# Optimization experiments

Measured on AMD Instinct MI355X. Metric: run time of the kernel, lower is better.

Reference implementation:

```python
import jax, jax.numpy as jnp
import numpy as np

B, C, H, W = 8, 192, 128, 128
NH, WS, PS = 6, 8, 8
HD = C // NH
SCALE = HD ** -0.5

def _rel_pos_log(ws):
    # log-spaced signed relative coordinates, [N, N, 2]
    coords = np.stack(np.meshgrid(np.arange(ws), np.arange(ws), indexing='ij'))
    cf = coords.reshape(2, -1)
    rp = (cf[:, :, None] - cf[:, None, :]).transpose(1, 2, 0).astype(np.float32)
    return jnp.asarray(np.sign(rp) * np.log1p(np.abs(rp)))

def setup_inputs() -> dict:
    key = jax.random.key(0)
    ks = jax.random.split(key, 8)
    s = 0.02
    return {
        'x': jax.random.normal(ks[0], (B, C, H, W), jnp.float32),
        'V_w': jax.random.normal(ks[1], (C, C), jnp.float32) * s,
        'V_b': jnp.zeros((C,), jnp.float32),
        'QK_w': jax.random.normal(ks[2], (2 * C, C), jnp.float32) * s,
        'QK_b': jnp.zeros((2 * C,), jnp.float32),
        'proj_w': jax.random.normal(ks[3], (C, C), jnp.float32) * s,
        'proj_b': jnp.zeros((C,), jnp.float32),
        'meta_w1': jax.random.normal(ks[4], (2, 256), jnp.float32) * s,
        'meta_b1': jnp.zeros((256,), jnp.float32),
        'meta_w2': jax.random.normal(ks[5], (256, NH), jnp.float32) * s,
        'meta_b2': jnp.zeros((NH,), jnp.float32),
    }

def reference(x, V_w, V_b, QK_w, QK_b, proj_w, proj_b, meta_w1, meta_b1, meta_w2, meta_b2):
    N = WS * WS
    # 1x1 convs for V and QK
    v = jnp.einsum('bchw,oc->bohw', x, V_w) + V_b[None, :, None, None]
    qk = jnp.einsum('bchw,oc->bohw', x, QK_w) + QK_b[None, :, None, None]
    qkv = jnp.concatenate([qk, v], axis=1)  # [B, 3C, H, W]
    # window partition -> [B * nW, N, 3C]
    t = qkv.transpose(0, 2, 3, 1).reshape(B, H // WS, WS, W // WS, WS, 3 * C)
    wins = t.transpose(0, 1, 3, 2, 4, 5).reshape(-1, N, 3 * C)
    B_ = wins.shape[0]
    qkv3 = wins.reshape(B_, N, 3, NH, HD).transpose(2, 0, 3, 1, 4)
    q, k, vv = qkv3[0] * SCALE, qkv3[1], qkv3[2]  # [B_, NH, N, HD]
    # FFT cross-modulation of q and k over the 8x8 window grid (c = N/64 = 1)
    cg = N // (PS * PS)
    qp = q.reshape(B_, NH, cg, PS, PS, HD).transpose(0, 1, 2, 5, 3, 4)
    kp = k.reshape(B_, NH, cg, PS, PS, HD).transpose(0, 1, 2, 5, 3, 4)
    o = jnp.fft.irfft2(jnp.fft.rfft2(qp) * jnp.fft.rfft2(kp), s=(PS, PS))
    o = o.transpose(0, 1, 2, 4, 5, 3).reshape(B_, NH, N, HD)
    # relative position bias from meta MLP on log-spaced coords
    rp = _rel_pos_log(WS)  # [N, N, 2]
    bias = jax.nn.relu(rp @ meta_w1 + meta_b1) @ meta_w2 + meta_b2  # [N, N, NH]
    bias = bias.transpose(2, 0, 1)  # [NH, N, N]
    attn = jnp.einsum('bhnd,bhmd->bhnm', o, vv) + bias[None]
    attn = jax.nn.softmax(attn, axis=-1)
    y = jnp.einsum('bhnm,bhmd->bhnd', attn, vv).transpose(0, 2, 1, 3).reshape(B_, N, C)
    # window reverse -> [B, C, H, W]
    y = y.reshape(B, H // WS, W // WS, WS, WS, C).transpose(0, 1, 3, 2, 4, 5).reshape(B, H, W, C)
    y = y.transpose(0, 3, 1, 2)
    return jnp.einsum('bchw,oc->bohw', y, proj_w) + proj_b[None, :, None, None]
```

## Files before the change

### kernel.cpp

```cpp
#include <hip/hip_runtime.h>

#define SCALEQ 0.17677669529663687f

typedef __bf16 bf16x8 __attribute__((ext_vector_type(8)));
typedef float f32x4 __attribute__((ext_vector_type(4)));
typedef float f32x2 __attribute__((ext_vector_type(2)));

__device__ __forceinline__ float bflo(unsigned int u) { return __uint_as_float(u << 16); }
__device__ __forceinline__ float bfhi(unsigned int u) { return __uint_as_float(u & 0xffff0000u); }
__device__ __forceinline__ f32x2 b2x2(unsigned int u) {
    f32x2 r; r[0] = bflo(u); r[1] = bfhi(u); return r;
}
__device__ __forceinline__ unsigned short f2b(float f) {
    unsigned int u = __float_as_uint(f);
    u += 0x7fffu + ((u >> 16) & 1u);
    return (unsigned short)(u >> 16);
}

#define BUF0   0
#define QOFF   24576
#define KOFF   49152
#define POFF   24576
#define VOFF   73728
#define VTOFF  98304
#define BTOFF  122880
#define LDS_BYTES 128280

#define WS_WQKV_ELEMS 110592
#define WS_WP_OFF_EL  110592
#define WS_BT_OFF_B   294912

__device__ __forceinline__ bf16x8 ldsf(const char* p) {
    uint4 u = *(const uint4*)p;
    return __builtin_bit_cast(bf16x8, u);
}
__device__ __forceinline__ bf16x8 gldf(const unsigned short* p) {
    uint4 u = *(const uint4*)p;
    return __builtin_bit_cast(bf16x8, u);
}

__global__ void wprep_kernel(const float* __restrict__ QKw, const float* __restrict__ Vw,
                             const float* __restrict__ Pw, unsigned short* __restrict__ wsb) {
    int i = blockIdx.x * 256 + threadIdx.x;
    if (i >= 147456) return;
    if (i < WS_WQKV_ELEMS) {
        int r = i / 192, c = i - r * 192;
        float v = (r < 384) ? QKw[r * 192 + c] : Vw[(r - 384) * 192 + c];
        wsb[i] = f2b(v);
    } else {
        int j = i - WS_WQKV_ELEMS;
        wsb[WS_WP_OFF_EL + j] = f2b(Pw[j]);
    }
}

__global__ void bias_table_kernel(const float* __restrict__ Mw1, const float* __restrict__ Mb1,
                                  const float* __restrict__ Mw2, const float* __restrict__ Mb2,
                                  float* __restrict__ bias_out) {
    int t = blockIdx.x * 64 + threadIdx.x;
    if (t >= 225) return;
    int dyi = t / 15, dxi = t % 15;
    float dy = (float)(dyi - 7), dx = (float)(dxi - 7);
    float f0 = copysignf(log1pf(fabsf(dy)), dy);
    float f1 = copysignf(log1pf(fabsf(dx)), dx);
    float a0 = Mb2[0], a1 = Mb2[1], a2 = Mb2[2], a3 = Mb2[3], a4 = Mb2[4], a5 = Mb2[5];
    for (int u = 0; u < 256; ++u) {
        float hv = fmaxf(f0 * Mw1[u] + f1 * Mw1[256 + u] + Mb1[u], 0.0f);
        const float* w2 = Mw2 + u * 6;
        a0 = fmaf(hv, w2[0], a0); a1 = fmaf(hv, w2[1], a1);
        a2 = fmaf(hv, w2[2], a2); a3 = fmaf(hv, w2[3], a3);
        a4 = fmaf(hv, w2[4], a4); a5 = fmaf(hv, w2[5], a5);
    }
    float* bt = bias_out + t * 6;
    bt[0] = a0; bt[1] = a1; bt[2] = a2; bt[3] = a3; bt[4] = a4; bt[5] = a5;
}

__global__ __launch_bounds__(512, 2)
void fused_win_attn(const float* __restrict__ x,
                    const float* __restrict__ Vb, const float* __restrict__ QKb,
                    const float* __restrict__ Pb,
                    const unsigned short* __restrict__ wqkv,
                    const unsigned short* __restrict__ wp,
                    const float* __restrict__ bias_g,
                    float* __restrict__ out)
{
    extern __shared__ char smem[];
    const int t   = threadIdx.x;
    const int wv  = t >> 6;
    const int l15 = t & 15;
    const int l4  = (t >> 4) & 3;

    const int wid = ((blockIdx.x & 7) << 8) | (blockIdx.x >> 3);
    const int b   = wid >> 8;
    const int wy  = (wid >> 4) & 15;
    const int wx  = wid & 15;
    const int y0  = wy * 8, x0 = wx * 8;

    const f32x4 zz = {0.0f, 0.0f, 0.0f, 0.0f};

    {
        float* bt = (float*)(smem + BTOFF);
        for (int i = t; i < 1350; i += 512) bt[i] = bias_g[i];
    }

    {
        const float* xb = x + (size_t)b * 192 * 16384;
        #pragma unroll
        for (int i = 0; i < 6; ++i) {
            int idx = t + 512 * i;
            int c = idx >> 4, sub = idx & 15;
            int r = sub >> 1, hf = sub & 1;
            float4 v4 = *(const float4*)(xb + c * 16384 + (y0 + r) * 128 + x0 + hf * 4);
            int n0 = r * 8 + hf * 4;
            unsigned short sv[4] = {f2b(v4.x), f2b(v4.y), f2b(v4.z), f2b(v4.w)};
            #pragma unroll
            for (int e = 0; e < 4; ++e) {
                int n = n0 + e;
                *(unsigned short*)(smem + BUF0 + ((n * 384 + c * 2) ^ ((n & 7) << 4))) = sv[e];
            }
        }
    }
    __syncthreads();

    {
        const int wcol = wv & 3, wrow = wv >> 2;
        bf16x8 afr[6][2];
        #pragma unroll
        for (int ks = 0; ks < 6; ++ks)
            #pragma unroll
            for (int mtl = 0; mtl < 2; ++mtl) {
                int row = (wrow * 2 + mtl) * 16 + l15;
                afr[ks][mtl] = ldsf(smem + BUF0 + ((row * 384 + ks * 64 + l4 * 16) ^ ((row & 7) << 4)));
            }
        #pragma unroll
        for (int chunk = 0; chunk < 3; ++chunk) {
            bf16x8 bw[3][6];
            #pragma unroll
            for (int j = 0; j < 3; ++j) {
                int ob = wcol * 144 + chunk * 48 + j * 16;
                const unsigned short* wr = wqkv + (size_t)(ob + l15) * 192 + l4 * 8;
                #pragma unroll
                for (int ks = 0; ks < 6; ++ks) bw[j][ks] = gldf(wr + ks * 32);
            }
            f32x4 acc[3][2];
            #pragma unroll
            for (int j = 0; j < 3; ++j) { acc[j][0] = zz; acc[j][1] = zz; }
            #pragma unroll
            for (int ks = 0; ks < 6; ++ks)
                #pragma unroll
                for (int j = 0; j < 3; ++j)
                    #pragma unroll
                    for (int mtl = 0; mtl < 2; ++mtl)
                        acc[j][mtl] = __builtin_amdgcn_mfma_f32_16x16x32_bf16(afr[ks][mtl], bw[j][ks], acc[j][mtl], 0, 0, 0);
            #pragma unroll
            for (int j = 0; j < 3; ++j) {
                int ob  = wcol * 144 + chunk * 48 + j * 16;
                int och = ob + l15;
                float bv = (ob < 384) ? QKb[och] : Vb[och - 384];
                #pragma unroll
                for (int mtl = 0; mtl < 2; ++mtl) {
                    #pragma unroll
                    for (int rr = 0; rr < 4; ++rr) {
                        float val = acc[j][mtl][rr] + bv;
                        int tok = (wrow * 2 + mtl) * 16 + l4 * 4 + rr;
                        if (ob < 192) {
                            *(unsigned short*)(smem + QOFF + ((tok * 384 + och * 2) ^ ((tok & 7) << 4))) = f2b(val * SCALEQ);
                        } else if (ob < 384) {
                            int ch = och - 192;
                            *(unsigned short*)(smem + KOFF + ((tok * 384 + ch * 2) ^ ((tok & 7) << 4))) = f2b(val);
                        } else {
                            int ch = och - 384;
                            unsigned short hv = f2b(val);
                            *(unsigned short*)(smem + VOFF  + ((tok * 384 + ch * 2) ^ ((tok & 7) << 4))) = hv;
                            *(unsigned short*)(smem + VTOFF + ((ch * 128 + tok * 2) ^ ((ch & 7) << 4))) = hv;
                        }
                    }
                }
            }
        }
    }
    __syncthreads();

    if (t < 384) {
        const int rn = t / 48, cc = t % 48;
        const int c0b = cc * 8;
        f32x2 acc[8][2];
        #pragma unroll
        for (int cn = 0; cn < 8; ++cn) {
            acc[cn][0] = (f32x2){0.0f, 0.0f};
            acc[cn][1] = (f32x2){0.0f, 0.0f};
        }

        #pragma unroll
        for (int kh = 0; kh < 2; ++kh) {
            uint2 karr[32];
            #pragma unroll
            for (int m = 0; m < 32; ++m) {
                int row = kh * 32 + m;
                karr[m] = *(const uint2*)(smem + KOFF + ((row * 384 + c0b) ^ ((row & 7) << 4)));
            }
            #pragma unroll
            for (int mrl = 0; mrl < 4; ++mrl) {
                const int mr = kh * 4 + mrl;
                f32x2 kf[8][2];
                #pragma unroll
                for (int mc = 0; mc < 8; ++mc) {
                    uint2 kv = karr[mrl * 8 + mc];
                    kf[mc][0] = b2x2(kv.x); kf[mc][1] = b2x2(kv.y);
                }
                const int npr = (rn - mr) & 7;
                #pragma unroll
                for (int npc = 0; npc < 8; ++npc) {
                    int np = npr * 8 + npc;
                    uint2 qv = *(const uint2*)(smem + QOFF + ((np * 384 + c0b) ^ ((np & 7) << 4)));
                    f32x2 qf0 = b2x2(qv.x), qf1 = b2x2(qv.y);
                    #pragma unroll
                    for (int mc = 0; mc < 8; ++mc) {
                        int cn = (npc + mc) & 7;
                        acc[cn][0] = qf0 * kf[mc][0] + acc[cn][0];
                        acc[cn][1] = qf1 * kf[mc][1] + acc[cn][1];
                    }
                }
            }
        }
        #pragma unroll
        for (int cn = 0; cn < 8; ++cn) {
            int n = rn * 8 + cn;
            uint2 pk;
            pk.x = (unsigned int)f2b(acc[cn][0][0]) | ((unsigned int)f2b(acc[cn][0][1]) << 16);
            pk.y = (unsigned int)f2b(acc[cn][1][0]) | ((unsigned int)f2b(acc[cn][1][1]) << 16);
            *(uint2*)(smem + BUF0 + ((n * 384 + c0b) ^ ((n & 7) << 4))) = pk;
        }
    }
    __syncthreads();

    {
        const float* bt = (const float*)(smem + BTOFF);
        for (int i = 0; i < 3; ++i) {
            int u = wv * 3 + i;
            int h = u >> 2, mt = u & 3;
            int arow = mt * 16 + l15;
            bf16x8 afr = ldsf(smem + BUF0 + ((arow * 384 + h * 64 + l4 * 16) ^ ((arow & 7) << 4)));
            f32x4 acc[4];
            #pragma unroll
            for (int nt = 0; nt < 4; ++nt) {
                int brow = nt * 16 + l15;
                bf16x8 bfr = ldsf(smem + VOFF + ((brow * 384 + h * 64 + l4 * 16) ^ ((brow & 7) << 4)));
                acc[nt] = __builtin_amdgcn_mfma_f32_16x16x32_bf16(afr, bfr, zz, 0, 0, 0);
            }
            float s[4][4];
            #pragma unroll
            for (int nt = 0; nt < 4; ++nt) {
                int m = nt * 16 + l15;
                int myr = m >> 3, myc = m & 7;
                #pragma unroll
                for (int rr = 0; rr < 4; ++rr) {
                    int n = mt * 16 + l4 * 4 + rr;
                    int dy = (n >> 3) - myr + 7, dx = (n & 7) - myc + 7;
                    s[nt][rr] = acc[nt][rr] + bt[(dy * 15 + dx) * 6 + h];
                }
            }
            float inv[4];
            #pragma unroll
            for (int rr = 0; rr < 4; ++rr) {
                float m0 = fmaxf(fmaxf(s[0][rr], s[1][rr]), fmaxf(s[2][rr], s[3][rr]));
                m0 = fmaxf(m0, __shfl_xor(m0, 1));
                m0 = fmaxf(m0, __shfl_xor(m0, 2));
                m0 = fmaxf(m0, __shfl_xor(m0, 4));
                m0 = fmaxf(m0, __shfl_xor(m0, 8));
                float sm = 0.0f;
                #pragma unroll
                for (int nt = 0; nt < 4; ++nt) {
                    float p = __expf(s[nt][rr] - m0);
                    s[nt][rr] = p; sm += p;
                }
                sm += __shfl_xor(sm, 1); sm += __shfl_xor(sm, 2);
                sm += __shfl_xor(sm, 4); sm += __shfl_xor(sm, 8);
                inv[rr] = 1.0f / sm;
            }
            #pragma unroll
            for (int nt = 0; nt < 4; ++nt)
                #pragma unroll
                for (int rr = 0; rr < 4; ++rr) {
                    int n = mt * 16 + l4 * 4 + rr, m = nt * 16 + l15;
                    *(unsigned short*)(smem + POFF + h * 8192 + ((n * 128 + m * 2) ^ ((n & 7) << 4)))
                        = f2b(s[nt][rr] * inv[rr]);
                }
        }
    }
    __syncthreads();

    {
        for (int i = 0; i < 3; ++i) {
            int u = wv * 3 + i;
            int h = u >> 2, mt = u & 3;
            bf16x8 pa[2];
            #pragma unroll
            for (int ks = 0; ks < 2; ++ks) {
                int row = mt * 16 + l15;
                pa[ks] = ldsf(smem + POFF + h * 8192 + ((row * 128 + ks * 64 + l4 * 16) ^ ((row & 7) << 4)));
            }
            f32x4 acc[2];
            acc[0] = zz; acc[1] = zz;
            #pragma unroll
            for (int dt = 0; dt < 2; ++dt)
                #pragma unroll
                for (int ks = 0; ks < 2; ++ks) {
                    int ch = h * 32 + dt * 16 + l15;
                    bf16x8 bfr = ldsf(smem + VTOFF + ((ch * 128 + ks * 64 + l4 * 16) ^ ((ch & 7) << 4)));
                    acc[dt] = __builtin_amdgcn_mfma_f32_16x16x32_bf16(pa[ks], bfr, acc[dt], 0, 0, 0);
                }
            #pragma unroll
            for (int dt = 0; dt < 2; ++dt)
                #pragma unroll
                for (int rr = 0; rr < 4; ++rr) {
                    int tok = mt * 16 + l4 * 4 + rr;
                    int ch  = h * 32 + dt * 16 + l15;
                    *(unsigned short*)(smem + BUF0 + ((tok * 384 + ch * 2) ^ ((tok & 7) << 4))) = f2b(acc[dt][rr]);
                }
        }
    }
    __syncthreads();

    {
        const int wc = wv & 3, wr = wv >> 2;
        bf16x8 wfr[3][6];
        #pragma unroll
        for (int jt = 0; jt < 3; ++jt) {
            int oc = wc * 48 + jt * 16;
            const unsigned short* wr_ = wp + (size_t)(oc + l15) * 192 + l4 * 8;
            #pragma unroll
            for (int ks = 0; ks < 6; ++ks) wfr[jt][ks] = gldf(wr_ + ks * 32);
        }
        f32x4 acc[3][2];
        #pragma unroll
        for (int jt = 0; jt < 3; ++jt) { acc[jt][0] = zz; acc[jt][1] = zz; }

        #pragma unroll
        for (int ks = 0; ks < 6; ++ks) {
            bf16x8 bfr[2];
            #pragma unroll
            for (int ntl = 0; ntl < 2; ++ntl) {
                int tok = (wr * 2 + ntl) * 16 + l15;
                bfr[ntl] = ldsf(smem + BUF0 + ((tok * 384 + ks * 64 + l4 * 16) ^ ((tok & 7) << 4)));
            }
            #pragma unroll
            for (int jt = 0; jt < 3; ++jt)
                #pragma unroll
                for (int ntl = 0; ntl < 2; ++ntl)
                    acc[jt][ntl] = __builtin_amdgcn_mfma_f32_16x16x32_bf16(wfr[jt][ks], bfr[ntl], acc[jt][ntl], 0, 0, 0);
        }
        #pragma unroll
        for (int jt = 0; jt < 3; ++jt)
            #pragma unroll
            for (int rr = 0; rr < 4; ++rr) {
                int oc = wc * 48 + jt * 16 + l4 * 4 + rr;
                float pb = Pb[oc];
                float* obase = out + (size_t)(b * 192 + oc) * 16384;
                #pragma unroll
                for (int ntl = 0; ntl < 2; ++ntl) {
                    int tok = (wr * 2 + ntl) * 16 + l15;
                    obase[(y0 + (tok >> 3)) * 128 + x0 + (tok & 7)] = acc[jt][ntl][rr] + pb;
                }
            }
    }
}

extern "C" void kernel_launch(void* const* d_in, const int* in_sizes, int n_in,
                              void* d_out, int out_size, void* d_ws, size_t ws_size,
                              hipStream_t stream) {
    const float* x   = (const float*)d_in[0];
    const float* Vw  = (const float*)d_in[1];
    const float* Vb  = (const float*)d_in[2];
    const float* QKw = (const float*)d_in[3];
    const float* QKb = (const float*)d_in[4];
    const float* Pw  = (const float*)d_in[5];
    const float* Pb  = (const float*)d_in[6];
    const float* Mw1 = (const float*)d_in[7];
    const float* Mb1 = (const float*)d_in[8];
    const float* Mw2 = (const float*)d_in[9];
    const float* Mb2 = (const float*)d_in[10];
    float* outp = (float*)d_out;

    unsigned short* wsb  = (unsigned short*)d_ws;
    float* biasw = (float*)((char*)d_ws + WS_BT_OFF_B);

    wprep_kernel<<<dim3(576), dim3(256), 0, stream>>>(QKw, Vw, Pw, wsb);
    bias_table_kernel<<<dim3(4), dim3(64), 0, stream>>>(Mw1, Mb1, Mw2, Mb2, biasw);

    (void)hipFuncSetAttribute((const void*)fused_win_attn,
                              hipFuncAttributeMaxDynamicSharedMemorySize, LDS_BYTES);
    fused_win_attn<<<dim3(2048), dim3(512), LDS_BYTES, stream>>>(
        x, Vb, QKb, Pb, wsb, wsb + WS_WP_OFF_EL, biasw, outp);
}
```

Before: 333.7 us.

## Shrink LDS footprint via buffer aliasing and register-resident P/V to double occupancy

```diff
diff --git a/kernel.cpp b/kernel.cpp
--- a/kernel.cpp
+++ b/kernel.cpp
@@ -16,15 +16,15 @@
     u += 0x7fffu + ((u >> 16) & 1u);
     return (unsigned short)(u >> 16);
 }
-
-#define BUF0   0
-#define QOFF   24576
-#define KOFF   49152
-#define POFF   24576
-#define VOFF   73728
-#define VTOFF  98304
-#define BTOFF  122880
-#define LDS_BYTES 128280
+__device__ __forceinline__ unsigned int pk2(float a, float b) {
+    return (unsigned int)f2b(a) | ((unsigned int)f2b(b) << 16);
+}
+
+#define RA     0
+#define RB     24576
+#define RC     49152
+#define BTOFF  73728
+#define LDS_BYTES 79128
 
 #define WS_WQKV_ELEMS 110592
 #define WS_WP_OFF_EL  110592
@@ -74,7 +74,7 @@
     bt[0] = a0; bt[1] = a1; bt[2] = a2; bt[3] = a3; bt[4] = a4; bt[5] = a5;
 }
 
-__global__ __launch_bounds__(512, 2)
+__global__ __launch_bounds__(512, 4)
 void fused_win_attn(const float* __restrict__ x,
                     const float* __restrict__ Vb, const float* __restrict__ QKb,
                     const float* __restrict__ Pb,
@@ -115,33 +115,33 @@
             #pragma unroll
             for (int e = 0; e < 4; ++e) {
                 int n = n0 + e;
-                *(unsigned short*)(smem + BUF0 + ((n * 384 + c * 2) ^ ((n & 7) << 4))) = sv[e];
-            }
-        }
-    }
-    __syncthreads();
-
-    {
-        const int wcol = wv & 3, wrow = wv >> 2;
+                *(unsigned short*)(smem + RA + ((n * 384 + c * 2) ^ ((n & 7) << 4))) = sv[e];
+            }
+        }
+    }
+    __syncthreads();
+
+    const int wcol = wv & 3, wrow = wv >> 2;
+    unsigned int vp[3][2][2];
+    {
         bf16x8 afr[6][2];
         #pragma unroll
         for (int ks = 0; ks < 6; ++ks)
             #pragma unroll
             for (int mtl = 0; mtl < 2; ++mtl) {
                 int row = (wrow * 2 + mtl) * 16 + l15;
-                afr[ks][mtl] = ldsf(smem + BUF0 + ((row * 384 + ks * 64 + l4 * 16) ^ ((row & 7) << 4)));
-            }
-        #pragma unroll
-        for (int chunk = 0; chunk < 3; ++chunk) {
+                afr[ks][mtl] = ldsf(smem + RA + ((row * 384 + ks * 64 + l4 * 16) ^ ((row & 7) << 4)));
+            }
+        __syncthreads();
+
+        auto gemm3 = [&](int obase, f32x4 acc[3][2]) {
             bf16x8 bw[3][6];
             #pragma unroll
             for (int j = 0; j < 3; ++j) {
-                int ob = wcol * 144 + chunk * 48 + j * 16;
-                const unsigned short* wr = wqkv + (size_t)(ob + l15) * 192 + l4 * 8;
+                const unsigned short* wr = wqkv + (size_t)(obase + j * 16 + l15) * 192 + l4 * 8;
                 #pragma unroll
                 for (int ks = 0; ks < 6; ++ks) bw[j][ks] = gldf(wr + ks * 32);
             }
-            f32x4 acc[3][2];
             #pragma unroll
             for (int j = 0; j < 3; ++j) { acc[j][0] = zz; acc[j][1] = zz; }
             #pragma unroll
@@ -151,29 +151,53 @@
                     #pragma unroll
                     for (int mtl = 0; mtl < 2; ++mtl)
                         acc[j][mtl] = __builtin_amdgcn_mfma_f32_16x16x32_bf16(afr[ks][mtl], bw[j][ks], acc[j][mtl], 0, 0, 0);
+        };
+
+        {
+            f32x4 acc[3][2];
+            gemm3(wcol * 48, acc);
             #pragma unroll
             for (int j = 0; j < 3; ++j) {
-                int ob  = wcol * 144 + chunk * 48 + j * 16;
-                int och = ob + l15;
-                float bv = (ob < 384) ? QKb[och] : Vb[och - 384];
-                #pragma unroll
-                for (int mtl = 0; mtl < 2; ++mtl) {
+                int och = wcol * 48 + j * 16 + l15;
+                float bv = QKb[och];
+                #pragma unroll
+                for (int mtl = 0; mtl < 2; ++mtl)
                     #pragma unroll
                     for (int rr = 0; rr < 4; ++rr) {
-                        float val = acc[j][mtl][rr] + bv;
                         int tok = (wrow * 2 + mtl) * 16 + l4 * 4 + rr;
-                        if (ob < 192) {
-                            *(unsigned short*)(smem + QOFF + ((tok * 384 + och * 2) ^ ((tok & 7) << 4))) = f2b(val * SCALEQ);
-                        } else if (ob < 384) {
-                            int ch = och - 192;
-                            *(unsigned short*)(smem + KOFF + ((tok * 384 + ch * 2) ^ ((tok & 7) << 4))) = f2b(val);
-                        } else {
-                            int ch = och - 384;
-                            unsigned short hv = f2b(val);
-                            *(unsigned short*)(smem + VOFF  + ((tok * 384 + ch * 2) ^ ((tok & 7) << 4))) = hv;
-                            *(unsigned short*)(smem + VTOFF + ((ch * 128 + tok * 2) ^ ((ch & 7) << 4))) = hv;
-                        }
+                        *(unsigned short*)(smem + RA + ((tok * 384 + och * 2) ^ ((tok & 7) << 4)))
+                            = f2b((acc[j][mtl][rr] + bv) * SCALEQ);
                     }
+            }
+        }
+        {
+            f32x4 acc[3][2];
+            gemm3(192 + wcol * 48, acc);
+            #pragma unroll
+            for (int j = 0; j < 3; ++j) {
+                int ch = wcol * 48 + j * 16 + l15;
+                float bv = QKb[192 + ch];
+                #pragma unroll
+                for (int mtl = 0; mtl < 2; ++mtl)
+                    #pragma unroll
+                    for (int rr = 0; rr < 4; ++rr) {
+                        int tok = (wrow * 2 + mtl) * 16 + l4 * 4 + rr;
+                        *(unsigned short*)(smem + RB + ((tok * 384 + ch * 2) ^ ((tok & 7) << 4)))
+                            = f2b(acc[j][mtl][rr] + bv);
+                    }
+            }
+        }
+        {
+            f32x4 acc[3][2];
+            gemm3(384 + wcol * 48, acc);
+            #pragma unroll
+            for (int j = 0; j < 3; ++j) {
+                int ch = wcol * 48 + j * 16 + l15;
+                float bv = Vb[ch];
+                #pragma unroll
+                for (int mtl = 0; mtl < 2; ++mtl) {
+                    vp[j][mtl][0] = pk2(acc[j][mtl][0] + bv, acc[j][mtl][1] + bv);
+                    vp[j][mtl][1] = pk2(acc[j][mtl][2] + bv, acc[j][mtl][3] + bv);
                 }
             }
         }
@@ -189,14 +213,13 @@
             acc[cn][0] = (f32x2){0.0f, 0.0f};
             acc[cn][1] = (f32x2){0.0f, 0.0f};
         }
-
         #pragma unroll
         for (int kh = 0; kh < 2; ++kh) {
             uint2 karr[32];
             #pragma unroll
             for (int m = 0; m < 32; ++m) {
                 int row = kh * 32 + m;
-                karr[m] = *(const uint2*)(smem + KOFF + ((row * 384 + c0b) ^ ((row & 7) << 4)));
+                karr[m] = *(const uint2*)(smem + RB + ((row * 384 + c0b) ^ ((row & 7) << 4)));
             }
             #pragma unroll
             for (int mrl = 0; mrl < 4; ++mrl) {
@@ -211,7 +234,7 @@
                 #pragma unroll
                 for (int npc = 0; npc < 8; ++npc) {
                     int np = npr * 8 + npc;
-                    uint2 qv = *(const uint2*)(smem + QOFF + ((np * 384 + c0b) ^ ((np & 7) << 4)));
+                    uint2 qv = *(const uint2*)(smem + RA + ((np * 384 + c0b) ^ ((np & 7) << 4)));
                     f32x2 qf0 = b2x2(qv.x), qf1 = b2x2(qv.y);
                     #pragma unroll
                     for (int mc = 0; mc < 8; ++mc) {
@@ -226,78 +249,103 @@
         for (int cn = 0; cn < 8; ++cn) {
             int n = rn * 8 + cn;
             uint2 pk;
-            pk.x = (unsigned int)f2b(acc[cn][0][0]) | ((unsigned int)f2b(acc[cn][0][1]) << 16);
-            pk.y = (unsigned int)f2b(acc[cn][1][0]) | ((unsigned int)f2b(acc[cn][1][1]) << 16);
-            *(uint2*)(smem + BUF0 + ((n * 384 + c0b) ^ ((n & 7) << 4))) = pk;
-        }
-    }
-    __syncthreads();
-
+            pk.x = pk2(acc[cn][0][0], acc[cn][0][1]);
+            pk.y = pk2(acc[cn][1][0], acc[cn][1][1]);
+            *(uint2*)(smem + RC + ((n * 384 + c0b) ^ ((n & 7) << 4))) = pk;
+        }
+    }
+    __syncthreads();
+
+    {
+        #pragma unroll
+        for (int j = 0; j < 3; ++j) {
+            int ch = wcol * 48 + j * 16 + l15;
+            #pragma unroll
+            for (int mtl = 0; mtl < 2; ++mtl)
+                #pragma unroll
+                for (int pp = 0; pp < 2; ++pp) {
+                    unsigned int pk = vp[j][mtl][pp];
+                    int tok0 = (wrow * 2 + mtl) * 16 + l4 * 4 + pp * 2;
+                    *(unsigned int*)(smem + RB + ((ch * 128 + tok0 * 2) ^ ((ch & 7) << 4))) = pk;
+                    *(unsigned short*)(smem + RA + ((tok0 * 384 + ch * 2) ^ ((tok0 & 7) << 4)))
+                        = (unsigned short)(pk & 0xffffu);
+                    *(unsigned short*)(smem + RA + (((tok0 + 1) * 384 + ch * 2) ^ (((tok0 + 1) & 7) << 4)))
+                        = (unsigned short)(pk >> 16);
+                }
+        }
+    }
+    __syncthreads();
+
+    unsigned int pv[3][4][2];
     {
         const float* bt = (const float*)(smem + BTOFF);
+        #pragma unroll
         for (int i = 0; i < 3; ++i) {
             int u = wv * 3 + i;
-            int h = u >> 2, mt = u & 3;
-            int arow = mt * 16 + l15;
-            bf16x8 afr = ldsf(smem + BUF0 + ((arow * 384 + h * 64 + l4 * 16) ^ ((arow & 7) << 4)));
-            f32x4 acc[4];
-            #pragma unroll
-            for (int nt = 0; nt < 4; ++nt) {
-                int brow = nt * 16 + l15;
-                bf16x8 bfr = ldsf(smem + VOFF + ((brow * 384 + h * 64 + l4 * 16) ^ ((brow & 7) << 4)));
-                acc[nt] = __builtin_amdgcn_mfma_f32_16x16x32_bf16(afr, bfr, zz, 0, 0, 0);
-            }
+            int h = u >> 2, nt = u & 3;
+            int brow = nt * 16 + l15;
+            bf16x8 ofr = ldsf(smem + RC + ((brow * 384 + h * 64 + l4 * 16) ^ ((brow & 7) << 4)));
+            int n = nt * 16 + l15;
+            int nr = n >> 3, nc = n & 7;
             float s[4][4];
             #pragma unroll
-            for (int nt = 0; nt < 4; ++nt) {
-                int m = nt * 16 + l15;
-                int myr = m >> 3, myc = m & 7;
+            for (int mt = 0; mt < 4; ++mt) {
+                int arow = mt * 16 + l15;
+                bf16x8 vfr = ldsf(smem + RA + ((arow * 384 + h * 64 + l4 * 16) ^ ((arow & 7) << 4)));
+                f32x4 a = __builtin_amdgcn_mfma_f32_16x16x32_bf16(vfr, ofr, zz, 0, 0, 0);
                 #pragma unroll
                 for (int rr = 0; rr < 4; ++rr) {
-                    int n = mt * 16 + l4 * 4 + rr;
-                    int dy = (n >> 3) - myr + 7, dx = (n & 7) - myc + 7;
-                    s[nt][rr] = acc[nt][rr] + bt[(dy * 15 + dx) * 6 + h];
-                }
-            }
-            float inv[4];
-            #pragma unroll
-            for (int rr = 0; rr < 4; ++rr) {
-                float m0 = fmaxf(fmaxf(s[0][rr], s[1][rr]), fmaxf(s[2][rr], s[3][rr]));
-                m0 = fmaxf(m0, __shfl_xor(m0, 1));
-                m0 = fmaxf(m0, __shfl_xor(m0, 2));
-                m0 = fmaxf(m0, __shfl_xor(m0, 4));
-                m0 = fmaxf(m0, __shfl_xor(m0, 8));
-                float sm = 0.0f;
-                #pragma unroll
-                for (int nt = 0; nt < 4; ++nt) {
-                    float p = __expf(s[nt][rr] - m0);
-                    s[nt][rr] = p; sm += p;
-                }
-                sm += __shfl_xor(sm, 1); sm += __shfl_xor(sm, 2);
-                sm += __shfl_xor(sm, 4); sm += __shfl_xor(sm, 8);
-                inv[rr] = 1.0f / sm;
-            }
-            #pragma unroll
-            for (int nt = 0; nt < 4; ++nt)
+                    int m = mt * 16 + l4 * 4 + rr;
+                    int dy = nr - (m >> 3) + 7, dx = nc - (m & 7) + 7;
+                    s[mt][rr] = a[rr] + bt[(dy * 15 + dx) * 6 + h];
+                }
+            }
+            float m0 = s[0][0];
+            #pragma unroll
+            for (int mt = 0; mt < 4; ++mt)
+                #pragma unroll
+                for (int rr = 0; rr < 4; ++rr) m0 = fmaxf(m0, s[mt][rr]);
+            m0 = fmaxf(m0, __shfl_xor(m0, 16));
+            m0 = fmaxf(m0, __shfl_xor(m0, 32));
+            float sm = 0.0f;
+            #pragma unroll
+            for (int mt = 0; mt < 4; ++mt)
                 #pragma unroll
                 for (int rr = 0; rr < 4; ++rr) {
-                    int n = mt * 16 + l4 * 4 + rr, m = nt * 16 + l15;
-                    *(unsigned short*)(smem + POFF + h * 8192 + ((n * 128 + m * 2) ^ ((n & 7) << 4)))
-                        = f2b(s[nt][rr] * inv[rr]);
-                }
-        }
-    }
-    __syncthreads();
-
-    {
+                    float p = __expf(s[mt][rr] - m0);
+                    s[mt][rr] = p; sm += p;
+                }
+            sm += __shfl_xor(sm, 16);
+            sm += __shfl_xor(sm, 32);
+            float inv = 1.0f / sm;
+            #pragma unroll
+            for (int mt = 0; mt < 4; ++mt) {
+                pv[i][mt][0] = pk2(s[mt][0] * inv, s[mt][1] * inv);
+                pv[i][mt][1] = pk2(s[mt][2] * inv, s[mt][3] * inv);
+            }
+        }
+    }
+    __syncthreads();
+
+    {
+        #pragma unroll
         for (int i = 0; i < 3; ++i) {
             int u = wv * 3 + i;
-            int h = u >> 2, mt = u & 3;
-            bf16x8 pa[2];
+            int h = u >> 2, nt = u & 3;
+            bf16x8 pafr[2];
             #pragma unroll
             for (int ks = 0; ks < 2; ++ks) {
-                int row = mt * 16 + l15;
-                pa[ks] = ldsf(smem + POFF + h * 8192 + ((row * 128 + ks * 64 + l4 * 16) ^ ((row & 7) << 4)));
+                unsigned int au[4];
+                #pragma unroll
+                for (int p = 0; p < 4; ++p) {
+                    int srcl4 = (2 * l4 + (p >> 1)) & 3;
+                    int src = srcl4 * 16 + l15;
+                    unsigned int v0 = (unsigned int)__shfl((int)pv[i][2 * ks][p & 1], src, 64);
+                    unsigned int v1 = (unsigned int)__shfl((int)pv[i][2 * ks + 1][p & 1], src, 64);
+                    au[p] = (l4 & 2) ? v1 : v0;
+                }
+                uint4 u4 = {au[0], au[1], au[2], au[3]};
+                pafr[ks] = __builtin_bit_cast(bf16x8, u4);
             }
             f32x4 acc[2];
             acc[0] = zz; acc[1] = zz;
@@ -305,17 +353,17 @@
             for (int dt = 0; dt < 2; ++dt)
                 #pragma unroll
                 for (int ks = 0; ks < 2; ++ks) {
-                    int ch = h * 32 + dt * 16 + l15;
-                    bf16x8 bfr = ldsf(smem + VTOFF + ((ch * 128 + ks * 64 + l4 * 16) ^ ((ch & 7) << 4)));
-                    acc[dt] = __builtin_amdgcn_mfma_f32_16x16x32_bf16(pa[ks], bfr, acc[dt], 0, 0, 0);
+                    int drow = h * 32 + dt * 16 + l15;
+                    bf16x8 vtf = ldsf(smem + RB + ((drow * 128 + ks * 64 + l4 * 16) ^ ((drow & 7) << 4)));
+                    acc[dt] = __builtin_amdgcn_mfma_f32_16x16x32_bf16(pafr[ks], vtf, acc[dt], 0, 0, 0);
                 }
             #pragma unroll
             for (int dt = 0; dt < 2; ++dt)
                 #pragma unroll
                 for (int rr = 0; rr < 4; ++rr) {
-                    int tok = mt * 16 + l4 * 4 + rr;
+                    int tok = nt * 16 + l4 * 4 + rr;
                     int ch  = h * 32 + dt * 16 + l15;
-                    *(unsigned short*)(smem + BUF0 + ((tok * 384 + ch * 2) ^ ((tok & 7) << 4))) = f2b(acc[dt][rr]);
+                    *(unsigned short*)(smem + RC + ((tok * 384 + ch * 2) ^ ((tok & 7) << 4))) = f2b(acc[dt][rr]);
                 }
         }
     }
@@ -341,7 +389,7 @@
             #pragma unroll
             for (int ntl = 0; ntl < 2; ++ntl) {
                 int tok = (wr * 2 + ntl) * 16 + l15;
-                bfr[ntl] = ldsf(smem + BUF0 + ((tok * 384 + ks * 64 + l4 * 16) ^ ((tok & 7) << 4)));
+                bfr[ntl] = ldsf(smem + RC + ((tok * 384 + ks * 64 + l4 * 16) ^ ((tok & 7) << 4)));
             }
             #pragma unroll
             for (int jt = 0; jt < 3; ++jt)
```

New measurement: 299.2 us. -10.3%, faster.
